# Kernel optimization log

Measured on AMD Instinct MI355X. Metric: run time of the kernel, lower is better.

## Reference

```python
import jax, jax.numpy as jnp
import numpy as np

N_GRAPHS = 32
N_NODES = 2048          # nodes per graph == lstm1 input_size
N_TOTAL = N_GRAPHS * N_NODES
N_EDGES = 1048576
HEADS = 8
GAT_OUT = 12            # per-head GAT output dim (== num_features)
OUT_CH = 9
NEG_SLOPE = 0.2
BN_EPS = 1e-5


def setup_inputs() -> dict:
    key = jax.random.key(0)
    ks = jax.random.split(key, 20)
    inp = {}
    inp['x'] = jax.random.normal(ks[0], (N_TOTAL, GAT_OUT), jnp.float32)
    inp['edge_index'] = jax.random.randint(ks[1], (2, N_EDGES), 0, N_TOTAL, jnp.int64)
    inp['W_gat'] = jax.random.normal(ks[2], (GAT_OUT, HEADS * GAT_OUT), jnp.float32) * 0.3
    inp['a_src'] = jax.random.normal(ks[3], (HEADS, GAT_OUT), jnp.float32) * 0.3
    inp['a_dst'] = jax.random.normal(ks[4], (HEADS, GAT_OUT), jnp.float32) * 0.3
    inp['gat_bias'] = jax.random.normal(ks[5], (GAT_OUT,), jnp.float32) * 0.1
    inp['bn_gamma'] = jax.random.uniform(ks[6], (GAT_OUT,), jnp.float32, 0.5, 1.5)
    inp['bn_beta'] = jax.random.normal(ks[7], (GAT_OUT,), jnp.float32) * 0.1
    inp['bn_mean'] = jax.random.normal(ks[8], (GAT_OUT,), jnp.float32) * 0.1
    inp['bn_var'] = jax.random.uniform(ks[9], (GAT_OUT,), jnp.float32, 0.5, 1.5)
    inp['w_ih1'] = jax.random.normal(ks[10], (4 * 32, N_NODES), jnp.float32) / np.sqrt(N_NODES)
    inp['w_hh1'] = jax.random.normal(ks[11], (4 * 32, 32), jnp.float32) / np.sqrt(32)
    inp['b_ih1'] = jnp.zeros((4 * 32,), jnp.float32)
    inp['b_hh1'] = jnp.zeros((4 * 32,), jnp.float32)
    inp['w_ih2'] = jax.random.normal(ks[12], (4 * 128, 32), jnp.float32) / np.sqrt(32)
    inp['w_hh2'] = jax.random.normal(ks[13], (4 * 128, 128), jnp.float32) / np.sqrt(128)
    inp['b_ih2'] = jnp.zeros((4 * 128,), jnp.float32)
    inp['b_hh2'] = jnp.zeros((4 * 128,), jnp.float32)
    inp['lin_w'] = jax.random.normal(ks[14], (N_NODES, 128), jnp.float32) / np.sqrt(128)
    inp['lin_b'] = jax.random.normal(ks[15], (N_NODES,), jnp.float32) * 0.1
    return inp


def _gat(x, edge_index, W, a_src, a_dst, bias):
    # PyG GATConv, heads=HEADS, out=GAT_OUT, concat=False (mean over heads), eval mode.
    N = x.shape[0]
    xp = (x @ W).reshape(N, HEADS, GAT_OUT)               # [N,H,C]
    loops = jnp.arange(N, dtype=edge_index.dtype)
    src = jnp.concatenate([edge_index[0], loops])
    dst = jnp.concatenate([edge_index[1], loops])
    asrc = jnp.einsum('nhc,hc->nh', xp, a_src)            # [N,H]
    adst = jnp.einsum('nhc,hc->nh', xp, a_dst)
    e = jax.nn.leaky_relu(asrc[src] + adst[dst], NEG_SLOPE)  # [E,H]
    m = jax.ops.segment_max(e, dst, num_segments=N)
    e = jnp.exp(e - m[dst])
    denom = jax.ops.segment_sum(e, dst, num_segments=N)
    alpha = e / (denom[dst] + 1e-16)
    msg = xp[src] * alpha[:, :, None]                     # [E,H,C]
    out = jax.ops.segment_sum(msg, dst, num_segments=N)   # [N,H,C]
    return out.mean(axis=1) + bias                        # concat=False -> head mean


def _lstm(x_seq, w_ih, w_hh, b_ih, b_hh):
    # x_seq: [T,B,I]; PyTorch gate order i,f,g,o.
    Hh = w_hh.shape[1]
    B = x_seq.shape[1]
    bias = b_ih + b_hh

    def step(carry, xt):
        h, c = carry
        gates = xt @ w_ih.T + h @ w_hh.T + bias
        i, f, g, o = jnp.split(gates, 4, axis=-1)
        c = jax.nn.sigmoid(f) * c + jax.nn.sigmoid(i) * jnp.tanh(g)
        h = jax.nn.sigmoid(o) * jnp.tanh(c)
        return (h, c), h

    init = (jnp.zeros((B, Hh), x_seq.dtype), jnp.zeros((B, Hh), x_seq.dtype))
    _, hs = jax.lax.scan(step, init, x_seq)
    return hs


def reference(x, edge_index, W_gat, a_src, a_dst, gat_bias,
              bn_gamma, bn_beta, bn_mean, bn_var,
              w_ih1, w_hh1, b_ih1, b_hh1,
              w_ih2, w_hh2, b_ih2, b_hh2,
              lin_w, lin_b):
    h = _gat(x, edge_index, W_gat, a_src, a_dst, gat_bias)          # [N,12]
    h = (h - bn_mean) / jnp.sqrt(bn_var + BN_EPS) * bn_gamma + bn_beta
    # dropout inactive in eval mode
    h = jax.nn.log_softmax(h, axis=1)
    h = h.reshape(N_GRAPHS, N_NODES, GAT_OUT)
    h = jnp.moveaxis(h, 2, 0)                                       # [T=12,B,n]
    h = _lstm(h, w_ih1, w_hh1, b_ih1, b_hh1)                        # [12,B,32]
    h = _lstm(h, w_ih2, w_hh2, b_ih2, b_hh2)                        # [12,B,128]
    h = h @ lin_w.T + lin_b                                         # [12,B,n]
    h = h[-OUT_CH:]                                                 # [9,B,n]
    h = jnp.moveaxis(h, 0, 2)                                       # [B,n,9]
    return h.reshape(N_GRAPHS * N_NODES, OUT_CH)
```

## Files before the change

### kernel.cpp

```cpp
#include <hip/hip_runtime.h>
#include <math.h>

#define N_EDGES_C 1048576
#define N_TOTAL_C 65536

typedef _Float16 h2v __attribute__((ext_vector_type(2)));
typedef int i4v __attribute__((ext_vector_type(4)));

#if defined(__has_builtin)
#if __has_builtin(__builtin_amdgcn_fdot2)
#define HAS_FDOT2 1
#endif
#if __has_builtin(__builtin_amdgcn_rcpf)
#define HAS_RCPF 1
#endif
#endif

__device__ __forceinline__ float fdot2(h2v a, h2v b, float c) {
#ifdef HAS_FDOT2
    return __builtin_amdgcn_fdot2(a, b, c, false);
#else
    return c + (float)a.x * (float)b.x + (float)a.y * (float)b.y;
#endif
}

__device__ __forceinline__ float fast_rcp(float x) {
#ifdef HAS_RCPF
    return __builtin_amdgcn_rcpf(x);
#else
    return 1.0f / x;
#endif
}
__device__ __forceinline__ float sigf(float x){ return fast_rcp(1.0f + __expf(-x)); }
__device__ __forceinline__ float tanh_fast(float x){ return fmaf(2.0f, fast_rcp(1.0f + __expf(-2.0f*x)), -1.0f); }
__device__ __forceinline__ float lrelu(float x){ return (x>=0.f)? x : 0.2f*x; }


__global__ void prep_kernel(const float* __restrict__ x, const float* __restrict__ Wg,
                            const float* __restrict__ a_src, const float* __restrict__ a_dst,
                            _Float16* __restrict__ xpp)
{
    int tid = threadIdx.x;
    __shared__ float Ws[12*96];
    __shared__ float as_s[96], ad_s[96];
    for (int i = tid; i < 1152; i += 256) Ws[i] = Wg[i];
    if (tid < 96) { as_s[tid] = a_src[tid]; ad_s[tid] = a_dst[tid]; }
    __syncthreads();
    int gid = blockIdx.x * 256 + tid;
    int n = gid >> 3;
    int h = gid & 7;
    const float4* xv = (const float4*)(x + (size_t)n * 12);
    float4 v0 = xv[0], v1 = xv[1], v2 = xv[2];
    float xr[12] = {v0.x,v0.y,v0.z,v0.w, v1.x,v1.y,v1.z,v1.w, v2.x,v2.y,v2.z,v2.w};
    float xp_[12];
    #pragma unroll
    for (int c = 0; c < 12; c++) {
        float acc = 0.f;
        #pragma unroll
        for (int k = 0; k < 12; k++) acc += xr[k] * Ws[k*96 + h*12 + c];
        xp_[c] = acc;
    }
    float sa = 0.f, sd = 0.f;
    #pragma unroll
    for (int c = 0; c < 12; c++) { sa += xp_[c]*as_s[h*12+c]; sd += xp_[c]*ad_s[h*12+c]; }
    union { _Float16 hh[16]; float ff[8]; float4 f4[2]; } s;
    #pragma unroll
    for (int c = 0; c < 12; c++) s.hh[c] = (_Float16)xp_[c];
    s.ff[6] = sa;
    s.ff[7] = sd;
    float4* o = (float4*)(xpp + (size_t)gid * 16);
    o[0] = s.f4[0];
    o[1] = s.f4[1];
}

__global__ __launch_bounds__(256)
void edge_hist(const int* __restrict__ ei, unsigned* __restrict__ cnt,
               unsigned* __restrict__ rank8)
{
    __shared__ unsigned hist[16384];
    int tid = threadIdx.x;
    int slice = blockIdx.x;
    for (int i = tid; i < 16384; i += 256) hist[i] = 0;
    __syncthreads();
    const i4v* dst4 = (const i4v*)(ei + N_EDGES_C) + slice*2048;
    for (int i = tid; i < 2048; i += 256) {
        i4v d = __builtin_nontemporal_load(&dst4[i]);
        int dd[4] = {d.x, d.y, d.z, d.w};
        unsigned packed = 0;
        #pragma unroll
        for (int j = 0; j < 4; j++) {
            int dj = dd[j];
            unsigned sh = (unsigned)(dj & 3) << 3;
            unsigned old = atomicAdd(&hist[dj >> 2], 1u << sh);
            packed |= ((old >> sh) & 0xffu) << (j*8);
        }
        __builtin_nontemporal_store(packed, &rank8[slice*2048 + i]);
    }
    __syncthreads();
    unsigned* cg = cnt + (size_t)slice*16384;
    for (int i = tid; i < 16384; i += 256) cg[i] = hist[i];
}

__global__ __launch_bounds__(128)
void slice_prefix(unsigned* __restrict__ cnt, int* __restrict__ rowptr,
                  int* __restrict__ chunksum)
{
    __shared__ int ss[128];
    int tid = threadIdx.x;
    int w = blockIdx.x*128 + tid;
    unsigned run = 0;
    unsigned* base = cnt + w;
    #pragma unroll 1
    for (int s = 0; s < 128; s += 32) {
        unsigned v[32];
        #pragma unroll
        for (int k = 0; k < 32; k++) v[k] = base[(size_t)(s+k)*16384];
        #pragma unroll
        for (int k = 0; k < 32; k++) {
            base[(size_t)(s+k)*16384] = run;
            run += v[k];
        }
    }
    int d0 = (int)(run & 255u), d1 = (int)((run >> 8) & 255u);
    int d2 = (int)((run >> 16) & 255u), d3 = (int)(run >> 24);
    int tsum = d0 + d1 + d2 + d3;
    ss[tid] = tsum;
    __syncthreads();
    for (int off = 1; off < 128; off <<= 1) {
        int t = (tid >= off) ? ss[tid - off] : 0;
        __syncthreads();
        ss[tid] += t;
        __syncthreads();
    }
    int ex = ss[tid] - tsum;
    int4 r;
    r.x = ex;
    r.y = ex + d0;
    r.z = ex + d0 + d1;
    r.w = ex + d0 + d1 + d2;
    ((int4*)rowptr)[w] = r;
    if (tid == 127) chunksum[blockIdx.x] = ss[127];
}

__global__ void scan_mid(const int* __restrict__ chunksum, int* __restrict__ chunkoff,
                         int* __restrict__ rowptr)
{
    __shared__ int ss[128];
    int tid = threadIdx.x;
    int v = chunksum[tid];
    ss[tid] = v;
    __syncthreads();
    for (int off = 1; off < 128; off <<= 1) {
        int t = (tid >= off) ? ss[tid - off] : 0;
        __syncthreads();
        ss[tid] += t;
        __syncthreads();
    }
    chunkoff[tid] = ss[tid] - v;
    if (tid == 127) rowptr[65536] = ss[127];
}

__global__ __launch_bounds__(128)
void scan_out(const int* __restrict__ chunkoff, int* __restrict__ rowptr)
{
    int w = blockIdx.x*128 + threadIdx.x;
    int off = chunkoff[blockIdx.x];
    int4 r = ((int4*)rowptr)[w];
    r.x += off; r.y += off; r.z += off; r.w += off;
    ((int4*)rowptr)[w] = r;
}

__global__ __launch_bounds__(256)
void edge_scatter(const int* __restrict__ ei, const unsigned* __restrict__ rank8,
                  const unsigned* __restrict__ cnt, const int* __restrict__ rowptr,
                  int* __restrict__ csr)
{
    __shared__ unsigned pos_s[2048];
    __shared__ int src_s[2048];
    int slice = blockIdx.x >> 2;
    int quar  = blockIdx.x & 3;
    int base = slice*2048 + quar*512;
    const i4v* dst4 = (const i4v*)(ei + N_EDGES_C);
    const i4v* src4 = (const i4v*)ei;
    const unsigned* cslice = cnt + (size_t)slice*16384;
    for (int i = threadIdx.x; i < 512; i += 256) {
        int idx = base + i;
        i4v d = __builtin_nontemporal_load(&dst4[idx]);
        i4v s = __builtin_nontemporal_load(&src4[idx]);
        unsigned r = __builtin_nontemporal_load(&rank8[idx]);
        int dd[4] = {d.x, d.y, d.z, d.w};
        int ss[4] = {s.x, s.y, s.z, s.w};
        #pragma unroll
        for (int j = 0; j < 4; j++) {
            int dj = dd[j];
            unsigned word = cslice[dj >> 2];
            int so = (int)((word >> ((unsigned)(dj & 3) << 3)) & 0xffu);
            int rk = (int)((r >> (j*8)) & 0xffu);
            unsigned pos = (unsigned)(rowptr[dj] + so + rk);
            pos_s[i*4 + j] = pos | ((unsigned)(dj >> 13) << 24);
            src_s[i*4 + j] = ss[j];
        }
    }
    __syncthreads();
    #pragma unroll 1
    for (unsigned g = 0; g < 8; g++) {
        for (int e = threadIdx.x; e < 2048; e += 256) {
            unsigned pw = pos_s[e];
            if ((pw >> 24) == g) csr[pw & 0xFFFFFFu] = src_s[e];
        }
    }
}

__global__ void gat_aggregate(const _Float16* __restrict__ xpp,
                              const int* __restrict__ rowptr, const int* __restrict__ csr_src,
                              const float* __restrict__ gat_bias, const float* __restrict__ bn_gamma,
                              const float* __restrict__ bn_beta, const float* __restrict__ bn_mean,
                              const float* __restrict__ bn_var, float* __restrict__ seq)
{
    int gid = blockIdx.x * 256 + threadIdx.x;
    int n = gid >> 3;
    int h = gid & 7;

    float acc[12];
    float adst_n, d;
    {
        const float4* p = (const float4*)(xpp + (size_t)n*128 + h*16);
        float4 f0 = p[0], f1 = p[1];
        adst_n = f1.w;
        float w = __expf(lrelu(f1.z + adst_n));
        d = w;
        h2v c0 = __builtin_bit_cast(h2v, f0.x), c1 = __builtin_bit_cast(h2v, f0.y);
        h2v c2 = __builtin_bit_cast(h2v, f0.z), c3 = __builtin_bit_cast(h2v, f0.w);
        h2v c4 = __builtin_bit_cast(h2v, f1.x), c5 = __builtin_bit_cast(h2v, f1.y);
        acc[0]=w*(float)c0.x; acc[1]=w*(float)c0.y; acc[2]=w*(float)c1.x; acc[3]=w*(float)c1.y;
        acc[4]=w*(float)c2.x; acc[5]=w*(float)c2.y; acc[6]=w*(float)c3.x; acc[7]=w*(float)c3.y;
        acc[8]=w*(float)c4.x; acc[9]=w*(float)c4.y; acc[10]=w*(float)c5.x; acc[11]=w*(float)c5.y;
    }

    auto accum = [&](float4 f0, float4 f1) {
        float w = __expf(lrelu(f1.z + adst_n));
        d += w;
        h2v c0 = __builtin_bit_cast(h2v, f0.x), c1 = __builtin_bit_cast(h2v, f0.y);
        h2v c2 = __builtin_bit_cast(h2v, f0.z), c3 = __builtin_bit_cast(h2v, f0.w);
        h2v c4 = __builtin_bit_cast(h2v, f1.x), c5 = __builtin_bit_cast(h2v, f1.y);
        acc[0]+=w*(float)c0.x; acc[1]+=w*(float)c0.y; acc[2]+=w*(float)c1.x; acc[3]+=w*(float)c1.y;
        acc[4]+=w*(float)c2.x; acc[5]+=w*(float)c2.y; acc[6]+=w*(float)c3.x; acc[7]+=w*(float)c3.y;
        acc[8]+=w*(float)c4.x; acc[9]+=w*(float)c4.y; acc[10]+=w*(float)c5.x; acc[11]+=w*(float)c5.y;
    };

    int beg = rowptr[n], end = rowptr[n+1];
    const _Float16* xh = xpp + (size_t)h * 16;
    int i = beg;
    for (; i + 4 <= end; i += 4) {
        int s0 = csr_src[i+0];
        int s1 = csr_src[i+1];
        int s2 = csr_src[i+2];
        int s3 = csr_src[i+3];
        const float4* p0 = (const float4*)(xh + (size_t)s0*128);
        const float4* p1 = (const float4*)(xh + (size_t)s1*128);
        const float4* p2 = (const float4*)(xh + (size_t)s2*128);
        const float4* p3 = (const float4*)(xh + (size_t)s3*128);
        float4 a0 = p0[0], b0 = p0[1];
        float4 a1 = p1[0], b1 = p1[1];
        float4 a2 = p2[0], b2 = p2[1];
        float4 a3 = p3[0], b3 = p3[1];
        accum(a0, b0);
        accum(a1, b1);
        accum(a2, b2);
        accum(a3, b3);
    }
    for (; i < end; i++) {
        int src = csr_src[i];
        const float4* p = (const float4*)(xh + (size_t)src*128);
        float4 f0 = p[0], f1 = p[1];
        accum(f0, f1);
    }

    float inv = 1.0f / (d + 1e-16f);
    float res[12];
    #pragma unroll
    for (int c = 0; c < 12; c++) {
        float v = acc[c] * inv;
        v += __shfl_xor(v, 1);
        v += __shfl_xor(v, 2);
        v += __shfl_xor(v, 4);
        res[c] = v * 0.125f;
    }
    if (h == 0) {
        float vals[12];
        float mx = -1e30f;
        #pragma unroll
        for (int c = 0; c < 12; c++) {
            float v = res[c] + gat_bias[c];
            v = (v - bn_mean[c]) * rsqrtf(bn_var[c] + 1e-5f) * bn_gamma[c] + bn_beta[c];
            vals[c] = v;
            mx = fmaxf(mx, v);
        }
        float sum = 0.f;
        #pragma unroll
        for (int c = 0; c < 12; c++) sum += __expf(vals[c] - mx);
        float lse = __logf(sum) + mx;
        #pragma unroll
        for (int c = 0; c < 12; c++) seq[(size_t)c * N_TOTAL_C + n] = vals[c] - lse;
    }
}

__global__ void gemm_x1(const float* __restrict__ A, const float* __restrict__ B,
                        float* __restrict__ C)
{
    __shared__ float As[32][33], Bs[32][33];
    const int K = 2048, N = 128;
    int tid = threadIdx.x;
    int tx = tid & 31, ty = tid >> 5;
    int bm = blockIdx.x * 32, bn = blockIdx.y * 32;
    int kbase = blockIdx.z * 128;
    float acc[4] = {0.f,0.f,0.f,0.f};
    for (int kk = 0; kk < 128; kk += 32) {
        int k0 = kbase + kk;
        #pragma unroll
        for (int i = 0; i < 4; i++) {
            int r = ty + i*8;
            As[r][tx] = A[(size_t)(bm + r) * K + k0 + tx];
            Bs[r][tx] = B[(size_t)(bn + r) * K + k0 + tx];
        }
        __syncthreads();
        #pragma unroll
        for (int k = 0; k < 32; k++) {
            float bv = Bs[tx][k];
            #pragma unroll
            for (int i = 0; i < 4; i++) acc[i] += As[ty + i*8][k] * bv;
        }
        __syncthreads();
    }
    #pragma unroll
    for (int i = 0; i < 4; i++)
        atomicAdd(&C[(size_t)(bm + ty + i*8) * N + bn + tx], acc[i]);
}

__global__ __launch_bounds__(512)
void lstm_fused(const float* __restrict__ X1, const float* __restrict__ w_hh1,
                const float* __restrict__ b_ih1, const float* __restrict__ b_hh1,
                const float* __restrict__ w_ih2, const float* __restrict__ w_hh2,
                const float* __restrict__ b_ih2, const float* __restrict__ b_hh2,
                float* __restrict__ H2)
{
    __shared__ float whh1[128*33];
    __shared__ float b1s[128];
    __shared__ float h1[32], c1[32];
    __shared__ __align__(16) _Float16 h1s[32];
    __shared__ __align__(16) _Float16 h2s[128];
    __shared__ float c2[128];
    __shared__ float g1s[128], g2s[512];
    int tid = threadIdx.x;
    int b = blockIdx.x;

    h2v whh[64];
    {
        const float2* wh = (const float2*)(w_hh2 + (size_t)tid * 128);
        #pragma unroll
        for (int k = 0; k < 64; k++) {
            float2 v = wh[k];
            h2v t; t.x = (_Float16)v.x; t.y = (_Float16)v.y;
            whh[k] = t;
        }
    }
    h2v wih[16];
    {
        const float2* wi = (const float2*)(w_ih2 + (size_t)tid * 32);
        #pragma unroll
        for (int k = 0; k < 16; k++) {
            float2 v = wi[k];
            h2v t; t.x = (_Float16)v.x; t.y = (_Float16)v.y;
            wih[k] = t;
        }
    }
    float b2 = b_ih2[tid] + b_hh2[tid];

    for (int i = tid; i < 128*32; i += 512) whh1[(i >> 5)*33 + (i & 31)] = w_hh1[i];
    if (tid < 128) b1s[tid] = b_ih1[tid] + b_hh1[tid];
    if (tid < 32)  { h1[tid] = 0.f; c1[tid] = 0.f; h1s[tid] = (_Float16)0.f; }
    if (tid < 128) { c2[tid] = 0.f; h2s[tid] = (_Float16)0.f; }

    float xv = 0.f;
    if (tid < 128) xv = X1[((size_t)0*32 + b)*128 + tid];
    __syncthreads();

    for (int t = 0; t < 12; t++) {
        float xv_next = 0.f;
        if (t < 11 && tid < 128) xv_next = X1[((size_t)(t+1)*32 + b)*128 + tid];

        float p0 = b2, p1 = 0.f, p2 = 0.f, p3 = 0.f;
        #pragma unroll
        for (int j = 0; j < 16; j++) {
            float4 f = ((const float4*)h2s)[j];
            p0 = fdot2(__builtin_bit_cast(h2v, f.x), whh[j*4+0], p0);
            p1 = fdot2(__builtin_bit_cast(h2v, f.y), whh[j*4+1], p1);
            p2 = fdot2(__builtin_bit_cast(h2v, f.z), whh[j*4+2], p2);
            p3 = fdot2(__builtin_bit_cast(h2v, f.w), whh[j*4+3], p3);
        }
        float acc2 = (p0 + p1) + (p2 + p3);

        if (tid < 128) {
            const float* wr = &whh1[tid * 33];
            float acc = xv + b1s[tid];
            #pragma unroll
            for (int k = 0; k < 32; k++) acc += h1[k] * wr[k];
            g1s[tid] = acc;
        }
        __syncthreads();
        if (tid < 32) {
            float ig = sigf(g1s[tid]), fg = sigf(g1s[32+tid]);
            float gg = tanh_fast(g1s[64+tid]), og = sigf(g1s[96+tid]);
            float cn = fg * c1[tid] + ig * gg;
            c1[tid] = cn;
            float hn = og * tanh_fast(cn);
            h1[tid] = hn;
            h1s[tid] = (_Float16)hn;
        }
        __syncthreads();
        {
            float q0 = 0.f, q1 = 0.f, q2 = 0.f, q3 = 0.f;
            #pragma unroll
            for (int j = 0; j < 4; j++) {
                float4 f = ((const float4*)h1s)[j];
                q0 = fdot2(__builtin_bit_cast(h2v, f.x), wih[j*4+0], q0);
                q1 = fdot2(__builtin_bit_cast(h2v, f.y), wih[j*4+1], q1);
                q2 = fdot2(__builtin_bit_cast(h2v, f.z), wih[j*4+2], q2);
                q3 = fdot2(__builtin_bit_cast(h2v, f.w), wih[j*4+3], q3);
            }
            g2s[tid] = acc2 + (q0 + q1) + (q2 + q3);
        }
        __syncthreads();
        if (tid < 128) {
            float ig = sigf(g2s[tid]), fg = sigf(g2s[128+tid]);
            float gg = tanh_fast(g2s[256+tid]), og = sigf(g2s[384+tid]);
            float cn = fg * c2[tid] + ig * gg;
            c2[tid] = cn;
            float hn = og * tanh_fast(cn);
            h2s[tid] = (_Float16)hn;
            if (t >= 3) H2[((size_t)t*32 + b)*128 + tid] = hn;
        }
        __syncthreads();
        xv = xv_next;
    }
}

__global__ void gemm_out(const float* __restrict__ A, const float* __restrict__ B,
                         const float* __restrict__ bias, float* __restrict__ out)
{
    __shared__ float As[32][33], Bs[32][33];
    const int K = 128;
    int tid = threadIdx.x;
    int tx = tid & 31, ty = tid >> 5;
    int bm = blockIdx.x * 32, bn = blockIdx.y * 32;
    float acc[4] = {0.f,0.f,0.f,0.f};
    for (int k0 = 0; k0 < K; k0 += 32) {
        #pragma unroll
        for (int i = 0; i < 4; i++) {
            int r = ty + i*8;
            As[r][tx] = A[(size_t)(bm + r) * K + k0 + tx];
            Bs[r][tx] = B[(size_t)(bn + r) * K + k0 + tx];
        }
        __syncthreads();
        #pragma unroll
        for (int kk = 0; kk < 32; kk++) {
            float bv = Bs[tx][kk];
            #pragma unroll
            for (int i = 0; i < 4; i++) acc[i] += As[ty + i*8][kk] * bv;
        }
        __syncthreads();
    }
    int j = blockIdx.x;
    int nn = bn + tx;
    float bv = bias[nn];
    #pragma unroll
    for (int i = 0; i < 4; i++) {
        int bb = ty + i*8;
        out[((size_t)bb * 2048 + nn) * 9 + j] = acc[i] + bv;
    }
}

extern "C" void kernel_launch(void* const* d_in, const int* in_sizes, int n_in,
                              void* d_out, int out_size, void* d_ws, size_t ws_size,
                              hipStream_t stream)
{
    const float* x        = (const float*)d_in[0];
    const int*   ei       = (const int*)  d_in[1];
    const float* W_gat    = (const float*)d_in[2];
    const float* a_src    = (const float*)d_in[3];
    const float* a_dst    = (const float*)d_in[4];
    const float* gat_bias = (const float*)d_in[5];
    const float* bn_gamma = (const float*)d_in[6];
    const float* bn_beta  = (const float*)d_in[7];
    const float* bn_mean  = (const float*)d_in[8];
    const float* bn_var   = (const float*)d_in[9];
    const float* w_ih1    = (const float*)d_in[10];
    const float* w_hh1    = (const float*)d_in[11];
    const float* b_ih1    = (const float*)d_in[12];
    const float* b_hh1    = (const float*)d_in[13];
    const float* w_ih2    = (const float*)d_in[14];
    const float* w_hh2    = (const float*)d_in[15];
    const float* b_ih2    = (const float*)d_in[16];
    const float* b_hh2    = (const float*)d_in[17];
    const float* lin_w    = (const float*)d_in[18];
    const float* lin_b    = (const float*)d_in[19];
    float* out = (float*)d_out;

    float* ws = (float*)d_ws;
    _Float16* xpp = (_Float16*)ws;
    float* seq  = ws + 4194304;
    float* X1   = seq + 786432;
    float* H2   = X1  + 49152;
    int* rowptr = (int*)(H2 + 49152);
    int* deg    = rowptr + 65544;
    unsigned* cnt = (unsigned*)(deg + 65536);
    unsigned* rank8 = cnt + 2097152;
    int* csr    = (int*)(rank8 + 262144);

    int* chunksum = deg;
    int* chunkoff = deg + 128;

    hipMemsetAsync(X1, 0, 49152 * sizeof(float), stream);
    prep_kernel <<<2048, 256, 0, stream>>>(x, W_gat, a_src, a_dst, xpp);
    edge_hist   <<<128, 256, 0, stream>>>(ei, cnt, rank8);
    slice_prefix<<<128, 128, 0, stream>>>(cnt, rowptr, chunksum);
    scan_mid    <<<1, 128, 0, stream>>>(chunksum, chunkoff, rowptr);
    scan_out    <<<128, 128, 0, stream>>>(chunkoff, rowptr);
    edge_scatter<<<512, 256, 0, stream>>>(ei, rank8, cnt, rowptr, csr);
    gat_aggregate<<<2048, 256, 0, stream>>>(xpp, rowptr, csr,
                                            gat_bias, bn_gamma, bn_beta, bn_mean, bn_var, seq);
    gemm_x1<<<dim3(12, 4, 16), 256, 0, stream>>>(seq, w_ih1, X1);
    lstm_fused<<<32, 512, 0, stream>>>(X1, w_hh1, b_ih1, b_hh1, w_ih2, w_hh2, b_ih2, b_hh2, H2);
    gemm_out<<<dim3(9, 64), 256, 0, stream>>>(H2 + 96*128, lin_w, lin_b, out);
}
```

Baseline: 243.9 us.

## Fuse prefix-scan kernels via grid atomic barrier, rotate count layout, shrink GEMM split-K

Merges slice_prefix, scan_mid and scan_out into one kernel. Each block publishes its chunk sum, spins on a global counter until all 128 blocks are done, then computes the global offsets locally, removing two kernel launches. The per-slice count array is stored with a per-slice rotation so the strided column reads in slice_prefix no longer hit the same memory channels. gemm_x1 split-K drops from 16 to 4 partitions, giving fewer atomic accumulations but less parallelism. The spin barrier assumes all 128 blocks are resident at the same time.

```diff
diff --git a/kernel.cpp b/kernel.cpp
--- a/kernel.cpp
+++ b/kernel.cpp
@@ -34,6 +34,8 @@
 __device__ __forceinline__ float sigf(float x){ return fast_rcp(1.0f + __expf(-x)); }
 __device__ __forceinline__ float tanh_fast(float x){ return fmaf(2.0f, fast_rcp(1.0f + __expf(-2.0f*x)), -1.0f); }
 __device__ __forceinline__ float lrelu(float x){ return (x>=0.f)? x : 0.2f*x; }
+
+#define CNT_ROT(s, w) ((size_t)(s)*16384 + (((unsigned)(w) + (unsigned)(s)*521u) & 16383u))
 
 
 __global__ void prep_kernel(const float* __restrict__ x, const float* __restrict__ Wg,
@@ -75,11 +77,12 @@
 
 __global__ __launch_bounds__(256)
 void edge_hist(const int* __restrict__ ei, unsigned* __restrict__ cnt,
-               unsigned* __restrict__ rank8)
+               unsigned* __restrict__ rank8, int* __restrict__ ctr)
 {
     __shared__ unsigned hist[16384];
     int tid = threadIdx.x;
     int slice = blockIdx.x;
+    if (slice == 0 && tid == 0) *ctr = 0;
     for (int i = tid; i < 16384; i += 256) hist[i] = 0;
     __syncthreads();
     const i4v* dst4 = (const i4v*)(ei + N_EDGES_C) + slice*2048;
@@ -97,27 +100,26 @@
         __builtin_nontemporal_store(packed, &rank8[slice*2048 + i]);
     }
     __syncthreads();
-    unsigned* cg = cnt + (size_t)slice*16384;
-    for (int i = tid; i < 16384; i += 256) cg[i] = hist[i];
+    for (int i = tid; i < 16384; i += 256) cnt[CNT_ROT(slice, i)] = hist[i];
 }
 
 __global__ __launch_bounds__(128)
 void slice_prefix(unsigned* __restrict__ cnt, int* __restrict__ rowptr,
-                  int* __restrict__ chunksum)
+                  int* __restrict__ chunksum, int* __restrict__ ctr)
 {
     __shared__ int ss[128];
     int tid = threadIdx.x;
-    int w = blockIdx.x*128 + tid;
+    int bid = blockIdx.x;
+    int w = bid*128 + tid;
     unsigned run = 0;
-    unsigned* base = cnt + w;
     #pragma unroll 1
     for (int s = 0; s < 128; s += 32) {
         unsigned v[32];
         #pragma unroll
-        for (int k = 0; k < 32; k++) v[k] = base[(size_t)(s+k)*16384];
+        for (int k = 0; k < 32; k++) v[k] = cnt[CNT_ROT(s+k, w)];
         #pragma unroll
         for (int k = 0; k < 32; k++) {
-            base[(size_t)(s+k)*16384] = run;
+            cnt[CNT_ROT(s+k, w)] = run;
             run += v[k];
         }
     }
@@ -133,22 +135,19 @@
         __syncthreads();
     }
     int ex = ss[tid] - tsum;
-    int4 r;
-    r.x = ex;
-    r.y = ex + d0;
-    r.z = ex + d0 + d1;
-    r.w = ex + d0 + d1 + d2;
-    ((int4*)rowptr)[w] = r;
-    if (tid == 127) chunksum[blockIdx.x] = ss[127];
-}
-
-__global__ void scan_mid(const int* __restrict__ chunksum, int* __restrict__ chunkoff,
-                         int* __restrict__ rowptr)
-{
-    __shared__ int ss[128];
-    int tid = threadIdx.x;
-    int v = chunksum[tid];
-    ss[tid] = v;
+
+    if (tid == 127) {
+        __hip_atomic_store(&chunksum[bid], ss[127], __ATOMIC_RELEASE, __HIP_MEMORY_SCOPE_AGENT);
+        atomicAdd(ctr, 1);
+    }
+    if (tid == 0) {
+        while (__hip_atomic_load(ctr, __ATOMIC_ACQUIRE, __HIP_MEMORY_SCOPE_AGENT) < 128)
+            __builtin_amdgcn_s_sleep(2);
+    }
+    __syncthreads();
+
+    int csv = __hip_atomic_load(&chunksum[tid], __ATOMIC_RELAXED, __HIP_MEMORY_SCOPE_AGENT);
+    ss[tid] = csv;
     __syncthreads();
     for (int off = 1; off < 128; off <<= 1) {
         int t = (tid >= off) ? ss[tid - off] : 0;
@@ -156,18 +155,14 @@
         ss[tid] += t;
         __syncthreads();
     }
-    chunkoff[tid] = ss[tid] - v;
-    if (tid == 127) rowptr[65536] = ss[127];
-}
-
-__global__ __launch_bounds__(128)
-void scan_out(const int* __restrict__ chunkoff, int* __restrict__ rowptr)
-{
-    int w = blockIdx.x*128 + threadIdx.x;
-    int off = chunkoff[blockIdx.x];
-    int4 r = ((int4*)rowptr)[w];
-    r.x += off; r.y += off; r.z += off; r.w += off;
+    int goff = (bid == 0) ? 0 : ss[bid-1];
+    int4 r;
+    r.x = ex + goff;
+    r.y = r.x + d0;
+    r.z = r.y + d1;
+    r.w = r.z + d2;
     ((int4*)rowptr)[w] = r;
+    if (bid == 0 && tid == 127) rowptr[65536] = ss[127];
 }
 
 __global__ __launch_bounds__(256)
@@ -182,7 +177,6 @@
     int base = slice*2048 + quar*512;
     const i4v* dst4 = (const i4v*)(ei + N_EDGES_C);
     const i4v* src4 = (const i4v*)ei;
-    const unsigned* cslice = cnt + (size_t)slice*16384;
     for (int i = threadIdx.x; i < 512; i += 256) {
         int idx = base + i;
         i4v d = __builtin_nontemporal_load(&dst4[idx]);
@@ -193,7 +187,7 @@
         #pragma unroll
         for (int j = 0; j < 4; j++) {
             int dj = dd[j];
-            unsigned word = cslice[dj >> 2];
+            unsigned word = cnt[CNT_ROT(slice, dj >> 2)];
             int so = (int)((word >> ((unsigned)(dj & 3) << 3)) & 0xffu);
             int rk = (int)((r >> (j*8)) & 0xffu);
             unsigned pos = (unsigned)(rowptr[dj] + so + rk);
@@ -313,9 +307,9 @@
     int tid = threadIdx.x;
     int tx = tid & 31, ty = tid >> 5;
     int bm = blockIdx.x * 32, bn = blockIdx.y * 32;
-    int kbase = blockIdx.z * 128;
+    int kbase = blockIdx.z * 512;
     float acc[4] = {0.f,0.f,0.f,0.f};
-    for (int kk = 0; kk < 128; kk += 32) {
+    for (int kk = 0; kk < 512; kk += 32) {
         int k0 = kbase + kk;
         #pragma unroll
         for (int i = 0; i < 4; i++) {
@@ -518,18 +512,16 @@
     int* csr    = (int*)(rank8 + 262144);
 
     int* chunksum = deg;
-    int* chunkoff = deg + 128;
+    int* ctr      = deg + 256;
 
     hipMemsetAsync(X1, 0, 49152 * sizeof(float), stream);
     prep_kernel <<<2048, 256, 0, stream>>>(x, W_gat, a_src, a_dst, xpp);
-    edge_hist   <<<128, 256, 0, stream>>>(ei, cnt, rank8);
-    slice_prefix<<<128, 128, 0, stream>>>(cnt, rowptr, chunksum);
-    scan_mid    <<<1, 128, 0, stream>>>(chunksum, chunkoff, rowptr);
-    scan_out    <<<128, 128, 0, stream>>>(chunkoff, rowptr);
+    edge_hist   <<<128, 256, 0, stream>>>(ei, cnt, rank8, ctr);
+    slice_prefix<<<128, 128, 0, stream>>>(cnt, rowptr, chunksum, ctr);
     edge_scatter<<<512, 256, 0, stream>>>(ei, rank8, cnt, rowptr, csr);
     gat_aggregate<<<2048, 256, 0, stream>>>(xpp, rowptr, csr,
                                             gat_bias, bn_gamma, bn_beta, bn_mean, bn_var, seq);
-    gemm_x1<<<dim3(12, 4, 16), 256, 0, stream>>>(seq, w_ih1, X1);
+    gemm_x1<<<dim3(12, 4, 4), 256, 0, stream>>>(seq, w_ih1, X1);
     lstm_fused<<<32, 512, 0, stream>>>(X1, w_hh1, b_ih1, b_hh1, w_ih2, w_hh2, b_ih2, b_hh2, H2);
     gemm_out<<<dim3(9, 64), 256, 0, stream>>>(H2 + 96*128, lin_w, lin_b, out);
 }
```

After: 259.5 us. 6.4% more time.
